# Kernel tuning notes

Measured on AMD Instinct MI355X. Metric: run time of the kernel, lower is better.

Reference implementation:

```python
import jax, jax.numpy as jnp
import numpy as np

# --- SLAYER hyperparameters (from netParams) ---
THETA = 10.0        # spike threshold
TAU_SR = 10.0       # SRM alpha-kernel time constant (ms)
TAU_RHO = 1.0       # surrogate-gradient width
SCALE_RHO = 1.0     # surrogate-gradient scale
TS = 1.0            # simulation step (ms)
T_SAMPLE = 300      # number of time steps
K_LEN = 64          # truncated SRM kernel length

N_BATCH, N_IN, N_HID, N_OUT = 128, 784, 410, 10


def srm_kernel():
    # SRM-alpha kernel eps(t) = (t/tau) * exp(1 - t/tau), sampled at Ts, eps(0)=0
    t = jnp.arange(K_LEN, dtype=jnp.float32) * TS
    return (t / TAU_SR) * jnp.exp(1.0 - t / TAU_SR)


def psp(x):
    # Causal FIR filtering along time: out[t] = sum_k eps[k] * x[t-k]
    # x: [N, C, T]
    n, c, t = x.shape
    kern = srm_kernel()
    lhs = x.reshape(n * c, 1, t)
    rhs = kern[::-1].reshape(1, 1, K_LEN)  # flip: conv_general_dilated is cross-correlation
    out = jax.lax.conv_general_dilated(
        lhs, rhs, window_strides=(1,), padding=[(K_LEN - 1, 0)],
        dimension_numbers=("NCH", "OIH", "NCH"))
    return out.reshape(n, c, t)


@jax.custom_vjp
def spike_fn(u):
    # Heaviside threshold with surrogate gradient rho(u) = (scale/tau) * exp(-|u-theta|/tau)
    return (u >= THETA).astype(u.dtype)

def _spike_fwd(u):
    return spike_fn(u), u

def _spike_bwd(u, g):
    return (g * (SCALE_RHO / TAU_RHO) * jnp.exp(-jnp.abs(u - THETA) / TAU_RHO),)

spike_fn.defvjp(_spike_fwd, _spike_bwd)


def setup_inputs() -> dict:
    key = jax.random.key(0)
    k1, k2, k3, k4 = jax.random.split(key, 4)
    img = jax.random.uniform(k1, (N_BATCH, N_IN), dtype=jnp.float32)
    rand_u = jax.random.uniform(k2, (N_BATCH, N_IN, T_SAMPLE), dtype=jnp.float32)
    W1 = jax.random.normal(k3, (N_HID, N_IN), dtype=jnp.float32)
    W2 = jax.random.normal(k4, (N_OUT, N_HID), dtype=jnp.float32)
    return {"img": img, "rand_u": rand_u, "W1": W1, "W2": W2}


def reference(img, rand_u, W1, W2):
    # Poisson spike encoding: spike whenever uniform noise < pixel intensity
    s0 = (rand_u < img[:, :, None]).astype(jnp.float32)        # [N, 784, T]
    # fc1 (dense over spatial features, shared over time) -> psp -> spike
    a1 = jnp.einsum("nit,oi->not", s0, W1)                     # [N, 410, T]
    s1 = spike_fn(psp(a1))
    # fc2 -> psp -> spike
    a2 = jnp.einsum("nht,oh->not", s1, W2)                     # [N, 10, T]
    s2 = spike_fn(psp(a2))
    return s2
```

## Files before the change

### kernel.cpp

```cpp
#include <hip/hip_runtime.h>
#include <cstdint>
#include <cstddef>

#define N_B 128
#define N_I 784
#define N_H 410
#define N_O 10
#define TT  300
#define KL  64
#define NW  26
#define NKS 13
#define NTILES 26
#define SSTR 448
#define NKS2 7
#define NDIG 4

typedef int v4i __attribute__((ext_vector_type(4)));

__device__ __forceinline__ uint32_t expand4(uint32_t v) {
  return (v * 0x00204081u) & 0x01010101u;
}

__global__ void k_pack(const float* __restrict__ rand_u, const float* __restrict__ img,
                       uint32_t* __restrict__ s0w) {
  int n = blockIdx.y;
  int t = blockIdx.x * 64 + threadIdx.x;
  if (t >= TT) return;
  const float* rb = rand_u + (size_t)n * N_I * TT + t;
  const float* ib = img + (size_t)n * N_I;
  uint32_t* dst = s0w + ((size_t)n * TT + t) * NW;
  #pragma unroll 1
  for (int w = 0; w < 25; ++w) {
    int ib32 = w * 32;
    float r[32];
    #pragma unroll
    for (int b = 0; b < 32; ++b) {
      int i = ib32 + b;
      r[b] = (i < N_I) ? rb[(size_t)i * TT] : 2.0f;
    }
    uint32_t bits = 0;
    #pragma unroll
    for (int b = 0; b < 32; ++b) {
      int i = ib32 + b;
      float p = (i < N_I) ? ib[i] : 0.0f;
      bits |= (r[b] < p ? 1u : 0u) << b;
    }
    dst[w] = bits;
  }
  dst[25] = 0;
}

__global__ void k_eps(double* __restrict__ epsb) {
  int k = threadIdx.x;
  if (k < KL) {
    double td = (double)k;
    double e = (td / 10.0) * exp(1.0 - td / 10.0);
    epsb[k] = e;
    epsb[KL + k] = e * (1.0 / 268435456.0);
  }
}

__global__ void k_bprep(const float* __restrict__ W1, v4i* __restrict__ Bf) {
  int bid  = blockIdx.x;
  int lane = threadIdx.x;
  int ks   = bid % NKS;
  int rest = bid / NKS;
  int nt   = rest % NTILES;
  int d    = rest / NTILES;
  int o     = nt * 16 + (lane & 15);
  int kbase = ks * 64 + (lane >> 4) * 16;
  uint32_t wds[4] = {0, 0, 0, 0};
  for (int j = 0; j < 16; ++j) {
    int k = kbase + j;
    int dig = 0;
    if (o < N_H && k < N_I) {
      double w = (double)W1[(size_t)o * N_I + k];
      int r = (int)llround(w * 268435456.0);
      for (int dd = 0; dd <= d; ++dd) {
        dig = (int)(int8_t)(uint8_t)(r & 255);
        r = (r - dig) >> 8;
      }
    }
    wds[j >> 2] |= ((uint32_t)(uint8_t)(int8_t)dig) << (8 * (j & 3));
  }
  v4i v; v[0] = (int)wds[0]; v[1] = (int)wds[1]; v[2] = (int)wds[2]; v[3] = (int)wds[3];
  Bf[(size_t)bid * 64 + lane] = v;
}

__global__ void k_bprep2(const float* __restrict__ W2, v4i* __restrict__ Bf2) {
  int bid  = blockIdx.x;
  int lane = threadIdx.x;
  int ks = bid % NKS2, d = bid / NKS2;
  int o     = lane & 15;
  int kbase = ks * 64 + (lane >> 4) * 16;
  uint32_t wds[4] = {0, 0, 0, 0};
  for (int j = 0; j < 16; ++j) {
    int k = kbase + j;
    int dig = 0;
    if (o < N_O && k < N_H) {
      double w = (double)W2[(size_t)o * N_H + k];
      int r = (int)llround(w * 268435456.0);
      for (int dd = 0; dd <= d; ++dd) {
        dig = (int)(int8_t)(uint8_t)(r & 255);
        r = (r - dig) >> 8;
      }
    }
    wds[j >> 2] |= ((uint32_t)(uint8_t)(int8_t)dig) << (8 * (j & 3));
  }
  v4i v; v[0] = (int)wds[0]; v[1] = (int)wds[1]; v[2] = (int)wds[2]; v[3] = (int)wds[3];
  Bf2[(size_t)bid * 64 + lane] = v;
}

__global__ __launch_bounds__(64) void k_fused(const uint32_t* __restrict__ s0w,
                                              const v4i* __restrict__ Bf,
                                              uint8_t* __restrict__ s1) {
  __shared__ double tile[2][64][17];
  __shared__ __attribute__((aligned(16))) uint8_t btile[64][16];
  int lane = threadIdx.x;
  int nt = blockIdx.x, n = blockIdx.y;
  int lrow = lane & 15, quad = lane >> 4;
  int wsel = quad >> 1, hsel = (quad & 1) * 16;
  const double q   = exp(-0.1);
  const double q64 = exp(-6.4);
  const double cS  = (exp(1.0) / 10.0) * (1.0 / 268435456.0);
  double s1a = 0.0, s2a = 0.0, s1b = 0.0, s2b = 0.0;
  const v4i* bb = Bf + (size_t)nt * NKS * 64 + lane;
  const size_t dstr = (size_t)NTILES * NKS * 64;
  const uint32_t* srow = s0w + (size_t)n * TT * NW;
  uint8_t* sbase = s1 + (size_t)n * TT * SSTR + nt * 16;

  for (int ch = 0; ch < 5; ++ch) {
    int t0 = ch * 64;
    v4i acc[4][NDIG];
    #pragma unroll
    for (int mt = 0; mt < 4; ++mt)
      #pragma unroll
      for (int d = 0; d < NDIG; ++d) { acc[mt][d][0]=0; acc[mt][d][1]=0; acc[mt][d][2]=0; acc[mt][d][3]=0; }

    v4i bcur[NDIG]; uint32_t acur[4];
    #pragma unroll
    for (int d = 0; d < NDIG; ++d) bcur[d] = bb[(size_t)d * dstr];
    #pragma unroll
    for (int mt = 0; mt < 4; ++mt) {
      int row = t0 + mt * 16 + lrow; if (row > TT - 1) row = TT - 1;
      acur[mt] = srow[(size_t)row * NW + wsel];
    }
    for (int ks = 0; ks < NKS; ++ks) {
      int ks2 = (ks + 1 < NKS) ? ks + 1 : ks;
      v4i bnxt[NDIG]; uint32_t anxt[4];
      #pragma unroll
      for (int d = 0; d < NDIG; ++d) bnxt[d] = bb[(size_t)d * dstr + ks2 * 64];
      #pragma unroll
      for (int mt = 0; mt < 4; ++mt) {
        int row = t0 + mt * 16 + lrow; if (row > TT - 1) row = TT - 1;
        anxt[mt] = srow[(size_t)row * NW + ks2 * 2 + wsel];
      }
      #pragma unroll
      for (int mt = 0; mt < 4; ++mt) {
        uint32_t h = (acur[mt] >> hsel) & 0xFFFFu;
        v4i af;
        af[0] = (int)expand4(h & 0xF);
        af[1] = (int)expand4((h >> 4) & 0xF);
        af[2] = (int)expand4((h >> 8) & 0xF);
        af[3] = (int)expand4((h >> 12) & 0xF);
        #pragma unroll
        for (int d = 0; d < NDIG; ++d)
          acc[mt][d] = __builtin_amdgcn_mfma_i32_16x16x64_i8(af, bcur[d], acc[mt][d], 0, 0, 0);
      }
      #pragma unroll
      for (int d = 0; d < NDIG; ++d) bcur[d] = bnxt[d];
      #pragma unroll
      for (int mt = 0; mt < 4; ++mt) acur[mt] = anxt[mt];
    }

    int tb = ch & 1;
    #pragma unroll
    for (int mt = 0; mt < 4; ++mt)
      #pragma unroll
      for (int r = 0; r < 4; ++r) {
        double v = (double)acc[mt][0][r]
                 + 256.0      * (double)acc[mt][1][r]
                 + 65536.0    * (double)acc[mt][2][r]
                 + 16777216.0 * (double)acc[mt][3][r];
        tile[tb][mt * 16 + quad * 4 + r][lrow] = v;
      }

    int jmax = TT - t0; if (jmax > 64) jmax = 64;
    if (lane < 16) {
      if (ch == 0) {
        for (int j = 0; j < jmax; ++j) {
          double xa = tile[0][j][lane];
          s2a = q * (s2a + s1a);
          s1a = q * s1a + xa;
          btile[j][lane] = (cS * s2a >= 10.0) ? 1 : 0;
        }
      } else {
        for (int j = 0; j < jmax; ++j) {
          double xb = tile[tb ^ 1][j][lane];
          double xa = tile[tb][j][lane];
          s2b = q * (s2b + s1b);
          s1b = q * s1b + xb;
          s2a = q * (s2a + s1a);
          s1a = q * s1a + xa;
          double y = cS * (s2a - q64 * (s2b + 64.0 * s1b));
          btile[j][lane] = (y >= 10.0) ? 1 : 0;
        }
      }
    }

    if (lane < jmax) {
      uint4 v = *(const uint4*)&btile[lane][0];
      *(uint4*)(sbase + (size_t)(t0 + lane) * SSTR) = v;
    }
  }
}

__global__ void k_gemm2m(const uint8_t* __restrict__ s1, const v4i* __restrict__ Bf2,
                         double* __restrict__ a2) {
  int tid = threadIdx.x;
  int wave = tid >> 6, lane = tid & 63;
  int m0 = (blockIdx.x * 4 + wave) * 16;
  int lrow = lane & 15, quad = lane >> 4;
  v4i acc[NDIG];
  #pragma unroll
  for (int d = 0; d < NDIG; ++d) { acc[d][0]=0; acc[d][1]=0; acc[d][2]=0; acc[d][3]=0; }
  const uint8_t* arow = s1 + (size_t)(m0 + lrow) * SSTR + quad * 16;
  for (int ks = 0; ks < NKS2; ++ks) {
    v4i af = *(const v4i*)(arow + ks * 64);
    #pragma unroll
    for (int d = 0; d < NDIG; ++d) {
      v4i bf = Bf2[(size_t)(d * NKS2 + ks) * 64 + lane];
      acc[d] = __builtin_amdgcn_mfma_i32_16x16x64_i8(af, bf, acc[d], 0, 0, 0);
    }
  }
  int o = lrow;
  if (o < N_O) {
    #pragma unroll
    for (int r = 0; r < 4; ++r) {
      int m = m0 + quad * 4 + r;
      int nn = m / TT;
      int t = m - nn * TT;
      double v = (double)acc[0][r]
               + 256.0      * (double)acc[1][r]
               + 65536.0    * (double)acc[2][r]
               + 16777216.0 * (double)acc[3][r];
      a2[((size_t)nn * N_O + o) * TT + t] = v;
    }
  }
}

__global__ void k_fir2(const double* __restrict__ a2, const double* __restrict__ epsb,
                       float* __restrict__ out) {
  int flat = blockIdx.x * 256 + threadIdx.x;
  if (flat >= N_B * N_O * TT) return;
  int t    = flat % TT;
  int rest = flat / TT;
  int o    = rest % N_O;
  int nn   = rest / N_O;
  const double* arow = a2 + ((size_t)nn * N_O + o) * TT;
  const double* epsS = epsb + KL;
  double u = 0.0;
  int kmax = (t < KL - 1) ? t : (KL - 1);
  for (int k = 0; k <= kmax; ++k) u += epsS[k] * arow[t - k];
  out[((size_t)nn * N_O + o) * TT + t] = (u >= 10.0) ? 1.0f : 0.0f;
}

extern "C" void kernel_launch(void* const* d_in, const int* in_sizes, int n_in,
                              void* d_out, int out_size, void* d_ws, size_t ws_size,
                              hipStream_t stream) {
  const float* img   = (const float*)d_in[0];
  const float* randu = (const float*)d_in[1];
  const float* W1    = (const float*)d_in[2];
  const float* W2    = (const float*)d_in[3];
  float* out = (float*)d_out;

  char* ws = (char*)d_ws;
  size_t off = 0;
  auto alloc = [&](size_t bytes) -> void* {
    void* p = ws + off;
    off = (off + bytes + 511) & ~(size_t)511;
    return p;
  };
  uint32_t* s0w  = (uint32_t*)alloc((size_t)N_B * TT * NW * sizeof(uint32_t));
  v4i*      Bf   = (v4i*)     alloc((size_t)NDIG * NTILES * NKS * 64 * 16);
  v4i*      Bf2  = (v4i*)     alloc((size_t)NDIG * NKS2 * 64 * 16);
  double*   epsb = (double*)  alloc(128 * sizeof(double));
  uint8_t*  s1   = (uint8_t*) alloc((size_t)N_B * TT * SSTR);
  double*   a2   = (double*)  alloc((size_t)N_B * N_O * TT * sizeof(double));
  if (off > ws_size) return;

  k_pack  <<<dim3(5, N_B), 64, 0, stream>>>(randu, img, s0w);
  k_eps   <<<dim3(1), 64, 0, stream>>>(epsb);
  k_bprep <<<dim3(NDIG * NTILES * NKS), 64, 0, stream>>>(W1, Bf);
  k_bprep2<<<dim3(NDIG * NKS2), 64, 0, stream>>>(W2, Bf2);

  k_fused <<<dim3(NTILES, N_B), 64, 0, stream>>>(s0w, Bf, s1);
  k_gemm2m<<<dim3(N_B * TT / 64), 256, 0, stream>>>(s1, Bf2, a2);
  k_fir2  <<<dim3((N_B * N_O * TT + 255) / 256), 256, 0, stream>>>(a2, epsb, out);
}
```

Before: 363.7 us.

## Restructure fused layer kernels: 4-wave blocks, parallel time-segment recurrence, fuse layer2 with FIR

The layer-1 fused kernel now uses 256-thread blocks where four waves each compute 80 time rows of the MFMA GEMM at once. The PSP recurrence is then split into four 75-step time segments, each warmed up over the preceding 63 steps, so that four lanes groups run in parallel instead of one serial 300-step loop. Layer 2 GEMM and its FIR/threshold are fused into one per-batch kernel using the same segmented recurrence, dropping the a2 buffer, eps kernel and direct FIR loop. The weight prep kernels are merged into one launch and s1 gets a tile-major layout; the segmented warm-up adds redundant recurrence work and may change rounding slightly.

```diff
diff --git a/kernel.cpp b/kernel.cpp
--- a/kernel.cpp
+++ b/kernel.cpp
@@ -11,9 +11,10 @@
 #define NW  26
 #define NKS 13
 #define NTILES 26
-#define SSTR 448
+#define NDIG 4
 #define NKS2 7
-#define NDIG 4
+#define S1_TILE 4800
+#define S1_NSTRIDE 134400
 
 typedef int v4i __attribute__((ext_vector_type(4)));
 
@@ -50,219 +51,227 @@
   dst[25] = 0;
 }
 
-__global__ void k_eps(double* __restrict__ epsb) {
-  int k = threadIdx.x;
-  if (k < KL) {
-    double td = (double)k;
-    double e = (td / 10.0) * exp(1.0 - td / 10.0);
-    epsb[k] = e;
-    epsb[KL + k] = e * (1.0 / 268435456.0);
-  }
-}
-
-__global__ void k_bprep(const float* __restrict__ W1, v4i* __restrict__ Bf) {
+__global__ void k_bprepall(const float* __restrict__ W1, const float* __restrict__ W2,
+                           v4i* __restrict__ Bf, v4i* __restrict__ Bf2) {
   int bid  = blockIdx.x;
   int lane = threadIdx.x;
-  int ks   = bid % NKS;
-  int rest = bid / NKS;
-  int nt   = rest % NTILES;
-  int d    = rest / NTILES;
-  int o     = nt * 16 + (lane & 15);
-  int kbase = ks * 64 + (lane >> 4) * 16;
-  uint32_t wds[4] = {0, 0, 0, 0};
-  for (int j = 0; j < 16; ++j) {
-    int k = kbase + j;
-    int dig = 0;
-    if (o < N_H && k < N_I) {
-      double w = (double)W1[(size_t)o * N_I + k];
-      int r = (int)llround(w * 268435456.0);
-      for (int dd = 0; dd <= d; ++dd) {
-        dig = (int)(int8_t)(uint8_t)(r & 255);
-        r = (r - dig) >> 8;
-      }
-    }
-    wds[j >> 2] |= ((uint32_t)(uint8_t)(int8_t)dig) << (8 * (j & 3));
-  }
-  v4i v; v[0] = (int)wds[0]; v[1] = (int)wds[1]; v[2] = (int)wds[2]; v[3] = (int)wds[3];
-  Bf[(size_t)bid * 64 + lane] = v;
-}
-
-__global__ void k_bprep2(const float* __restrict__ W2, v4i* __restrict__ Bf2) {
-  int bid  = blockIdx.x;
-  int lane = threadIdx.x;
-  int ks = bid % NKS2, d = bid / NKS2;
-  int o     = lane & 15;
-  int kbase = ks * 64 + (lane >> 4) * 16;
-  uint32_t wds[4] = {0, 0, 0, 0};
-  for (int j = 0; j < 16; ++j) {
-    int k = kbase + j;
-    int dig = 0;
-    if (o < N_O && k < N_H) {
-      double w = (double)W2[(size_t)o * N_H + k];
-      int r = (int)llround(w * 268435456.0);
-      for (int dd = 0; dd <= d; ++dd) {
-        dig = (int)(int8_t)(uint8_t)(r & 255);
-        r = (r - dig) >> 8;
-      }
-    }
-    wds[j >> 2] |= ((uint32_t)(uint8_t)(int8_t)dig) << (8 * (j & 3));
-  }
-  v4i v; v[0] = (int)wds[0]; v[1] = (int)wds[1]; v[2] = (int)wds[2]; v[3] = (int)wds[3];
-  Bf2[(size_t)bid * 64 + lane] = v;
-}
-
-__global__ __launch_bounds__(64) void k_fused(const uint32_t* __restrict__ s0w,
-                                              const v4i* __restrict__ Bf,
-                                              uint8_t* __restrict__ s1) {
-  __shared__ double tile[2][64][17];
-  __shared__ __attribute__((aligned(16))) uint8_t btile[64][16];
-  int lane = threadIdx.x;
+  if (bid < NDIG * NTILES * NKS) {
+    int ks   = bid % NKS;
+    int rest = bid / NKS;
+    int nt   = rest % NTILES;
+    int d    = rest / NTILES;
+    int o     = nt * 16 + (lane & 15);
+    int kbase = ks * 64 + (lane >> 4) * 16;
+    uint32_t wds[4] = {0, 0, 0, 0};
+    for (int j = 0; j < 16; ++j) {
+      int k = kbase + j;
+      int dig = 0;
+      if (o < N_H && k < N_I) {
+        double w = (double)W1[(size_t)o * N_I + k];
+        int r = (int)llround(w * 268435456.0);
+        for (int dd = 0; dd <= d; ++dd) {
+          dig = (int)(int8_t)(uint8_t)(r & 255);
+          r = (r - dig) >> 8;
+        }
+      }
+      wds[j >> 2] |= ((uint32_t)(uint8_t)(int8_t)dig) << (8 * (j & 3));
+    }
+    v4i v; v[0] = (int)wds[0]; v[1] = (int)wds[1]; v[2] = (int)wds[2]; v[3] = (int)wds[3];
+    Bf[(size_t)bid * 64 + lane] = v;
+  } else {
+    int b2 = bid - NDIG * NTILES * NKS;
+    int ks = b2 % NKS2, d = b2 / NKS2;
+    int o     = lane & 15;
+    int kbase = ks * 64 + (lane >> 4) * 16;
+    uint32_t wds[4] = {0, 0, 0, 0};
+    for (int j = 0; j < 16; ++j) {
+      int k = kbase + j;
+      int dig = 0;
+      if (o < N_O && k < N_H) {
+        double w = (double)W2[(size_t)o * N_H + k];
+        int r = (int)llround(w * 268435456.0);
+        for (int dd = 0; dd <= d; ++dd) {
+          dig = (int)(int8_t)(uint8_t)(r & 255);
+          r = (r - dig) >> 8;
+        }
+      }
+      wds[j >> 2] |= ((uint32_t)(uint8_t)(int8_t)dig) << (8 * (j & 3));
+    }
+    v4i v; v[0] = (int)wds[0]; v[1] = (int)wds[1]; v[2] = (int)wds[2]; v[3] = (int)wds[3];
+    Bf2[(size_t)b2 * 64 + lane] = v;
+  }
+}
+
+__global__ __launch_bounds__(256) void k_fused2(const uint32_t* __restrict__ s0w,
+                                                const v4i* __restrict__ Bf,
+                                                uint8_t* __restrict__ s1) {
+  __shared__ double tile[TT][17];
+  int tid = threadIdx.x;
+  int wave = tid >> 6, lane = tid & 63;
   int nt = blockIdx.x, n = blockIdx.y;
   int lrow = lane & 15, quad = lane >> 4;
   int wsel = quad >> 1, hsel = (quad & 1) * 16;
-  const double q   = exp(-0.1);
-  const double q64 = exp(-6.4);
-  const double cS  = (exp(1.0) / 10.0) * (1.0 / 268435456.0);
-  double s1a = 0.0, s2a = 0.0, s1b = 0.0, s2b = 0.0;
   const v4i* bb = Bf + (size_t)nt * NKS * 64 + lane;
   const size_t dstr = (size_t)NTILES * NKS * 64;
   const uint32_t* srow = s0w + (size_t)n * TT * NW;
-  uint8_t* sbase = s1 + (size_t)n * TT * SSTR + nt * 16;
-
-  for (int ch = 0; ch < 5; ++ch) {
-    int t0 = ch * 64;
-    v4i acc[4][NDIG];
-    #pragma unroll
-    for (int mt = 0; mt < 4; ++mt)
+
+  v4i acc[5][NDIG];
+  #pragma unroll
+  for (int mti = 0; mti < 5; ++mti)
+    #pragma unroll
+    for (int d = 0; d < NDIG; ++d) { acc[mti][d][0]=0; acc[mti][d][1]=0; acc[mti][d][2]=0; acc[mti][d][3]=0; }
+  int rowc[5];
+  #pragma unroll
+  for (int mti = 0; mti < 5; ++mti) {
+    int rr = wave * 80 + mti * 16 + lrow;
+    rowc[mti] = (rr > TT - 1) ? TT - 1 : rr;
+  }
+  v4i bcur[NDIG]; uint32_t acur[5];
+  #pragma unroll
+  for (int d = 0; d < NDIG; ++d) bcur[d] = bb[(size_t)d * dstr];
+  #pragma unroll
+  for (int mti = 0; mti < 5; ++mti) acur[mti] = srow[(size_t)rowc[mti] * NW + wsel];
+  for (int ks = 0; ks < NKS; ++ks) {
+    int ks2 = (ks + 1 < NKS) ? ks + 1 : ks;
+    v4i bnxt[NDIG]; uint32_t anxt[5];
+    #pragma unroll
+    for (int d = 0; d < NDIG; ++d) bnxt[d] = bb[(size_t)d * dstr + ks2 * 64];
+    #pragma unroll
+    for (int mti = 0; mti < 5; ++mti) anxt[mti] = srow[(size_t)rowc[mti] * NW + ks2 * 2 + wsel];
+    #pragma unroll
+    for (int mti = 0; mti < 5; ++mti) {
+      uint32_t h = (acur[mti] >> hsel) & 0xFFFFu;
+      v4i af;
+      af[0] = (int)expand4(h & 0xF);
+      af[1] = (int)expand4((h >> 4) & 0xF);
+      af[2] = (int)expand4((h >> 8) & 0xF);
+      af[3] = (int)expand4((h >> 12) & 0xF);
       #pragma unroll
-      for (int d = 0; d < NDIG; ++d) { acc[mt][d][0]=0; acc[mt][d][1]=0; acc[mt][d][2]=0; acc[mt][d][3]=0; }
-
-    v4i bcur[NDIG]; uint32_t acur[4];
-    #pragma unroll
-    for (int d = 0; d < NDIG; ++d) bcur[d] = bb[(size_t)d * dstr];
-    #pragma unroll
-    for (int mt = 0; mt < 4; ++mt) {
-      int row = t0 + mt * 16 + lrow; if (row > TT - 1) row = TT - 1;
-      acur[mt] = srow[(size_t)row * NW + wsel];
-    }
-    for (int ks = 0; ks < NKS; ++ks) {
-      int ks2 = (ks + 1 < NKS) ? ks + 1 : ks;
-      v4i bnxt[NDIG]; uint32_t anxt[4];
-      #pragma unroll
-      for (int d = 0; d < NDIG; ++d) bnxt[d] = bb[(size_t)d * dstr + ks2 * 64];
-      #pragma unroll
-      for (int mt = 0; mt < 4; ++mt) {
-        int row = t0 + mt * 16 + lrow; if (row > TT - 1) row = TT - 1;
-        anxt[mt] = srow[(size_t)row * NW + ks2 * 2 + wsel];
-      }
-      #pragma unroll
-      for (int mt = 0; mt < 4; ++mt) {
-        uint32_t h = (acur[mt] >> hsel) & 0xFFFFu;
-        v4i af;
-        af[0] = (int)expand4(h & 0xF);
-        af[1] = (int)expand4((h >> 4) & 0xF);
-        af[2] = (int)expand4((h >> 8) & 0xF);
-        af[3] = (int)expand4((h >> 12) & 0xF);
-        #pragma unroll
-        for (int d = 0; d < NDIG; ++d)
-          acc[mt][d] = __builtin_amdgcn_mfma_i32_16x16x64_i8(af, bcur[d], acc[mt][d], 0, 0, 0);
-      }
-      #pragma unroll
-      for (int d = 0; d < NDIG; ++d) bcur[d] = bnxt[d];
-      #pragma unroll
-      for (int mt = 0; mt < 4; ++mt) acur[mt] = anxt[mt];
-    }
-
-    int tb = ch & 1;
-    #pragma unroll
-    for (int mt = 0; mt < 4; ++mt)
-      #pragma unroll
-      for (int r = 0; r < 4; ++r) {
-        double v = (double)acc[mt][0][r]
-                 + 256.0      * (double)acc[mt][1][r]
-                 + 65536.0    * (double)acc[mt][2][r]
-                 + 16777216.0 * (double)acc[mt][3][r];
-        tile[tb][mt * 16 + quad * 4 + r][lrow] = v;
-      }
-
-    int jmax = TT - t0; if (jmax > 64) jmax = 64;
-    if (lane < 16) {
-      if (ch == 0) {
-        for (int j = 0; j < jmax; ++j) {
-          double xa = tile[0][j][lane];
-          s2a = q * (s2a + s1a);
-          s1a = q * s1a + xa;
-          btile[j][lane] = (cS * s2a >= 10.0) ? 1 : 0;
-        }
-      } else {
-        for (int j = 0; j < jmax; ++j) {
-          double xb = tile[tb ^ 1][j][lane];
-          double xa = tile[tb][j][lane];
-          s2b = q * (s2b + s1b);
-          s1b = q * s1b + xb;
-          s2a = q * (s2a + s1a);
-          s1a = q * s1a + xa;
-          double y = cS * (s2a - q64 * (s2b + 64.0 * s1b));
-          btile[j][lane] = (y >= 10.0) ? 1 : 0;
-        }
-      }
-    }
-
-    if (lane < jmax) {
-      uint4 v = *(const uint4*)&btile[lane][0];
-      *(uint4*)(sbase + (size_t)(t0 + lane) * SSTR) = v;
-    }
-  }
-}
-
-__global__ void k_gemm2m(const uint8_t* __restrict__ s1, const v4i* __restrict__ Bf2,
-                         double* __restrict__ a2) {
+      for (int d = 0; d < NDIG; ++d)
+        acc[mti][d] = __builtin_amdgcn_mfma_i32_16x16x64_i8(af, bcur[d], acc[mti][d], 0, 0, 0);
+    }
+    #pragma unroll
+    for (int d = 0; d < NDIG; ++d) bcur[d] = bnxt[d];
+    #pragma unroll
+    for (int mti = 0; mti < 5; ++mti) acur[mti] = anxt[mti];
+  }
+  #pragma unroll
+  for (int mti = 0; mti < 5; ++mti)
+    #pragma unroll
+    for (int r = 0; r < 4; ++r) {
+      int m = wave * 80 + mti * 16 + quad * 4 + r;
+      if (m < TT) {
+        double v = (double)acc[mti][0][r]
+                 + 256.0      * (double)acc[mti][1][r]
+                 + 65536.0    * (double)acc[mti][2][r]
+                 + 16777216.0 * (double)acc[mti][3][r];
+        tile[m][lrow] = v;
+      }
+    }
+  __syncthreads();
+
+  if (lane < 16) {
+    int g = wave;
+    int T0 = g * 75, T1 = T0 + 75;
+    int W = T0 - 63; if (W < 0) W = 0;
+    int tB = W + 64, tM = (tB < T1) ? tB : T1;
+    const double q   = exp(-0.1);
+    const double q64 = exp(-6.4);
+    const double cS  = (exp(1.0) / 10.0) * (1.0 / 268435456.0);
+    double s1a = 0.0, s2a = 0.0, s1b = 0.0, s2b = 0.0;
+    uint8_t* sb = s1 + (size_t)n * S1_NSTRIDE + (size_t)nt * S1_TILE + lane;
+    for (int t = W; t < T0; ++t) {
+      double xa = tile[t][lane];
+      s2a = q * (s2a + s1a);
+      s1a = q * s1a + xa;
+    }
+    for (int t = T0; t < tM; ++t) {
+      double xa = tile[t][lane];
+      s2a = q * (s2a + s1a);
+      s1a = q * s1a + xa;
+      sb[(size_t)t * 16] = (cS * s2a >= 10.0) ? 1 : 0;
+    }
+    for (int t = tM; t < T1; ++t) {
+      double xb = tile[t - 64][lane];
+      double xa = tile[t][lane];
+      s2b = q * (s2b + s1b);
+      s1b = q * s1b + xb;
+      s2a = q * (s2a + s1a);
+      s1a = q * s1a + xa;
+      double y = cS * (s2a - q64 * (s2b + 64.0 * s1b));
+      sb[(size_t)t * 16] = (y >= 10.0) ? 1 : 0;
+    }
+  }
+}
+
+__global__ __launch_bounds__(256) void k_l2f(const uint8_t* __restrict__ s1,
+                                             const v4i* __restrict__ Bf2,
+                                             float* __restrict__ out) {
+  __shared__ double tile2[TT][11];
   int tid = threadIdx.x;
   int wave = tid >> 6, lane = tid & 63;
-  int m0 = (blockIdx.x * 4 + wave) * 16;
+  int n = blockIdx.x;
   int lrow = lane & 15, quad = lane >> 4;
-  v4i acc[NDIG];
-  #pragma unroll
-  for (int d = 0; d < NDIG; ++d) { acc[d][0]=0; acc[d][1]=0; acc[d][2]=0; acc[d][3]=0; }
-  const uint8_t* arow = s1 + (size_t)(m0 + lrow) * SSTR + quad * 16;
-  for (int ks = 0; ks < NKS2; ++ks) {
-    v4i af = *(const v4i*)(arow + ks * 64);
-    #pragma unroll
-    for (int d = 0; d < NDIG; ++d) {
-      v4i bf = Bf2[(size_t)(d * NKS2 + ks) * 64 + lane];
-      acc[d] = __builtin_amdgcn_mfma_i32_16x16x64_i8(af, bf, acc[d], 0, 0, 0);
-    }
-  }
-  int o = lrow;
-  if (o < N_O) {
+  const uint8_t* s1n = s1 + (size_t)n * S1_NSTRIDE;
+  for (int mt = wave; mt < 19; mt += 4) {
+    int m0 = mt * 16;
+    int trow = m0 + lrow; if (trow > TT - 1) trow = TT - 1;
+    v4i acc[NDIG];
+    #pragma unroll
+    for (int d = 0; d < NDIG; ++d) { acc[d][0]=0; acc[d][1]=0; acc[d][2]=0; acc[d][3]=0; }
+    for (int ks = 0; ks < NKS2; ++ks) {
+      v4i af = *(const v4i*)(s1n + (size_t)(ks * 4 + quad) * S1_TILE + (size_t)trow * 16);
+      #pragma unroll
+      for (int d = 0; d < NDIG; ++d) {
+        v4i bf = Bf2[(size_t)(d * NKS2 + ks) * 64 + lane];
+        acc[d] = __builtin_amdgcn_mfma_i32_16x16x64_i8(af, bf, acc[d], 0, 0, 0);
+      }
+    }
     #pragma unroll
     for (int r = 0; r < 4; ++r) {
       int m = m0 + quad * 4 + r;
-      int nn = m / TT;
-      int t = m - nn * TT;
-      double v = (double)acc[0][r]
-               + 256.0      * (double)acc[1][r]
-               + 65536.0    * (double)acc[2][r]
-               + 16777216.0 * (double)acc[3][r];
-      a2[((size_t)nn * N_O + o) * TT + t] = v;
-    }
-  }
-}
-
-__global__ void k_fir2(const double* __restrict__ a2, const double* __restrict__ epsb,
-                       float* __restrict__ out) {
-  int flat = blockIdx.x * 256 + threadIdx.x;
-  if (flat >= N_B * N_O * TT) return;
-  int t    = flat % TT;
-  int rest = flat / TT;
-  int o    = rest % N_O;
-  int nn   = rest / N_O;
-  const double* arow = a2 + ((size_t)nn * N_O + o) * TT;
-  const double* epsS = epsb + KL;
-  double u = 0.0;
-  int kmax = (t < KL - 1) ? t : (KL - 1);
-  for (int k = 0; k <= kmax; ++k) u += epsS[k] * arow[t - k];
-  out[((size_t)nn * N_O + o) * TT + t] = (u >= 10.0) ? 1.0f : 0.0f;
+      if (m < TT && lrow < N_O) {
+        double v = (double)acc[0][r]
+                 + 256.0      * (double)acc[1][r]
+                 + 65536.0    * (double)acc[2][r]
+                 + 16777216.0 * (double)acc[3][r];
+        tile2[m][lrow] = v;
+      }
+    }
+  }
+  __syncthreads();
+  if (lane < N_O) {
+    int g = wave;
+    int T0 = g * 75, T1 = T0 + 75;
+    int W = T0 - 63; if (W < 0) W = 0;
+    int tB = W + 64, tM = (tB < T1) ? tB : T1;
+    const double q   = exp(-0.1);
+    const double q64 = exp(-6.4);
+    const double cS  = (exp(1.0) / 10.0) * (1.0 / 268435456.0);
+    double s1a = 0.0, s2a = 0.0, s1b = 0.0, s2b = 0.0;
+    float* ob = out + (size_t)n * N_O * TT + (size_t)lane * TT;
+    for (int t = W; t < T0; ++t) {
+      double xa = tile2[t][lane];
+      s2a = q * (s2a + s1a);
+      s1a = q * s1a + xa;
+    }
+    for (int t = T0; t < tM; ++t) {
+      double xa = tile2[t][lane];
+      s2a = q * (s2a + s1a);
+      s1a = q * s1a + xa;
+      ob[t] = (cS * s2a >= 10.0) ? 1.0f : 0.0f;
+    }
+    for (int t = tM; t < T1; ++t) {
+      double xb = tile2[t - 64][lane];
+      double xa = tile2[t][lane];
+      s2b = q * (s2b + s1b);
+      s1b = q * s1b + xb;
+      s2a = q * (s2a + s1a);
+      s1a = q * s1a + xa;
+      double y = cS * (s2a - q64 * (s2b + 64.0 * s1b));
+      ob[t] = (y >= 10.0) ? 1.0f : 0.0f;
+    }
+  }
 }
 
 extern "C" void kernel_launch(void* const* d_in, const int* in_sizes, int n_in,
@@ -281,20 +290,14 @@
     off = (off + bytes + 511) & ~(size_t)511;
     return p;
   };
-  uint32_t* s0w  = (uint32_t*)alloc((size_t)N_B * TT * NW * sizeof(uint32_t));
-  v4i*      Bf   = (v4i*)     alloc((size_t)NDIG * NTILES * NKS * 64 * 16);
-  v4i*      Bf2  = (v4i*)     alloc((size_t)NDIG * NKS2 * 64 * 16);
-  double*   epsb = (double*)  alloc(128 * sizeof(double));
-  uint8_t*  s1   = (uint8_t*) alloc((size_t)N_B * TT * SSTR);
-  double*   a2   = (double*)  alloc((size_t)N_B * N_O * TT * sizeof(double));
+  uint32_t* s0w = (uint32_t*)alloc((size_t)N_B * TT * NW * sizeof(uint32_t));
+  v4i*      Bf  = (v4i*)     alloc((size_t)NDIG * NTILES * NKS * 64 * 16);
+  v4i*      Bf2 = (v4i*)     alloc((size_t)NDIG * NKS2 * 64 * 16);
+  uint8_t*  s1  = (uint8_t*) alloc((size_t)N_B * S1_NSTRIDE);
   if (off > ws_size) return;
 
-  k_pack  <<<dim3(5, N_B), 64, 0, stream>>>(randu, img, s0w);
-  k_eps   <<<dim3(1), 64, 0, stream>>>(epsb);
-  k_bprep <<<dim3(NDIG * NTILES * NKS), 64, 0, stream>>>(W1, Bf);
-  k_bprep2<<<dim3(NDIG * NKS2), 64, 0, stream>>>(W2, Bf2);
-
-  k_fused <<<dim3(NTILES, N_B), 64, 0, stream>>>(s0w, Bf, s1);
-  k_gemm2m<<<dim3(N_B * TT / 64), 256, 0, stream>>>(s1, Bf2, a2);
-  k_fir2  <<<dim3((N_B * N_O * TT + 255) / 256), 256, 0, stream>>>(a2, epsb, out);
-}
+  k_pack    <<<dim3(5, N_B), 64, 0, stream>>>(randu, img, s0w);
+  k_bprepall<<<dim3(NDIG * NTILES * NKS + NDIG * NKS2), 64, 0, stream>>>(W1, W2, Bf, Bf2);
+  k_fused2  <<<dim3(NTILES, N_B), 256, 0, stream>>>(s0w, Bf, s1);
+  k_l2f     <<<dim3(N_B), 256, 0, stream>>>(s1, Bf2, out);
+}
```

Result: faster. 356.2 us (-2.1%).
